# Optimization experiments

Hardware: AMD Instinct MI355X
Metric: run time of the kernel (lower is better)

## Reference

```python
import jax, jax.numpy as jnp
import numpy as np

jax.config.update('jax_enable_x64', True)

NV = 300000
NT = 1200000

# Lookup tables from GshellHelper buffers
TRIANGLE_TABLE = jnp.asarray(np.array([
    [-1, -1, -1, -1, -1, -1], [1, 0, 2, -1, -1, -1], [4, 0, 3, -1, -1, -1],
    [1, 4, 2, 1, 3, 4], [3, 1, 5, -1, -1, -1], [2, 3, 0, 2, 5, 3],
    [1, 4, 0, 1, 5, 4], [4, 2, 5, -1, -1, -1], [4, 5, 2, -1, -1, -1],
    [4, 1, 0, 4, 5, 1], [3, 2, 0, 3, 5, 2], [1, 3, 5, -1, -1, -1],
    [4, 1, 2, 4, 3, 1], [3, 0, 4, -1, -1, -1], [2, 0, 1, -1, -1, -1],
    [-1, -1, -1, -1, -1, -1]], dtype=np.int64))
NUM_TRIANGLES_TABLE = jnp.asarray(np.array([0, 1, 1, 2, 1, 2, 2, 1, 1, 2, 2, 1, 2, 1, 1, 0], dtype=np.int64))
BASE_TET_EDGES = jnp.asarray(np.array([0, 1, 0, 2, 0, 3, 1, 2, 1, 3, 2, 3], dtype=np.int64))


def setup_inputs() -> dict:
    key = jax.random.key(0)
    k1, k2, k3 = jax.random.split(key, 3)
    pos_nx3 = jax.random.normal(k1, (NV, 3), dtype=jnp.float32)
    sdf_n = jax.random.normal(k2, (NV,), dtype=jnp.float32)
    tet_fx4 = jax.random.randint(k3, (NT, 4), 0, NV, dtype=jnp.int64)
    return {'pos_nx3': pos_nx3, 'sdf_n': sdf_n, 'tet_fx4': tet_fx4}


def _marching_tets(pos_nx3, sdf_n, tet_fx4):
    Nv = pos_nx3.shape[0]
    Nt = tet_fx4.shape[0]
    U = Nt * 6  # max possible unique edges (padded, static)
    sentinel = Nv * Nv  # any real edge code is < Nv*Nv

    occ_n = sdf_n > 0                               # [Nv]
    occ_fx4 = occ_n[tet_fx4]                        # [Nt,4]

    # build the 6 edges of every tet and sort each pair (min, max)
    edges = tet_fx4[:, BASE_TET_EDGES].reshape(-1, 2)   # [Nt*6, 2]
    e0 = jnp.minimum(edges[:, 0], edges[:, 1])
    e1 = jnp.maximum(edges[:, 0], edges[:, 1])
    code = e0 * Nv + e1                                  # [Nt*6] int64 edge key

    # dedup edges (torch.unique(..., return_inverse=True) equivalent, padded)
    uniq, inv = jnp.unique(code, size=U, fill_value=sentinel, return_inverse=True)
    u0 = jnp.clip(uniq // Nv, 0, Nv - 1)
    u1 = jnp.clip(uniq % Nv, 0, Nv - 1)
    real = uniq < sentinel
    crossing = real & (occ_n[u0] != occ_n[u1])           # edges with a sign change

    # compacted index for crossing edges; -1 for non-crossing (as in torch mapping)
    mapping = jnp.where(crossing, jnp.cumsum(crossing.astype(jnp.int64)) - 1, -1)
    idx_map = mapping[inv].reshape(Nt, 6)                # [Nt,6]

    # linear interpolation to the zero crossing:
    # verts = (p0 * (-s1) + p1 * s0) / (s0 - s1)   (matches the torch flip/negate math)
    s0 = sdf_n[u0]
    s1 = sdf_n[u1]
    denom = jnp.where(crossing, s0 - s1, jnp.asarray(1.0, sdf_n.dtype))
    v = (pos_nx3[u0] * (-s1 / denom)[:, None] + pos_nx3[u1] * (s0 / denom)[:, None])

    # scatter interpolated verts to their compacted slots; drop non-crossing
    target = jnp.where(crossing, mapping, U)
    verts = jnp.zeros((U, 3), pos_nx3.dtype).at[target].set(v, mode='drop')

    # per-tet sign pattern -> triangle table lookup
    v_id = jnp.asarray([1, 2, 4, 8], dtype=jnp.int64)
    tetindex = (occ_fx4.astype(jnp.int64) * v_id[None, :]).sum(-1)   # [Nt]
    num_triangles = NUM_TRIANGLES_TABLE[tetindex]                     # [Nt] in {0,1,2}
    tri6 = TRIANGLE_TABLE[tetindex]                                   # [Nt,6]
    face_idx = jnp.take_along_axis(idx_map, jnp.clip(tri6, 0, 5), axis=1).reshape(Nt, 2, 3)
    valid_tri = jnp.arange(2, dtype=jnp.int64)[None, :] < num_triangles[:, None]
    faces = jnp.where(valid_tri[:, :, None], face_idx, -1)            # [Nt,2,3], -1 padded

    return verts, faces, num_triangles, crossing


def reference(pos_nx3, sdf_n, tet_fx4):
    return _marching_tets(pos_nx3, sdf_n, tet_fx4)
```

## Files before the change

### kernel.cpp

```cpp
#include <hip/hip_runtime.h>
#include <stdint.h>

typedef unsigned long long u64;
typedef unsigned int u32;

#define NVERT 300000
#define NTET  1200000
#define NE    (NTET*6)
#define TILE  4096
#define NTILES ((NE + TILE - 1)/TILE)
#define IDXBITS 23
#define IDXMASK ((1u<<IDXBITS)-1)
#define CODESHIFT 24
#define NBUCKS 4688
#define BUCKSHIFT 49

#define PK_GRID 512

#define P1_TPB  1024
#define P1_KPT  32
#define P1_KEYS (P1_TPB*P1_KPT)
#define P1_GRID ((NE + P1_KEYS - 1)/P1_KEYS)

#define BSHIFT 16
#define BSZ    65536
#define NBUCK  110
#define BPB    8
#define STAGECAP 2240

#define VERTS_OFF 0
#define FACES_OFF 21600000
#define NUMT_OFF  28800000
#define CROSS_OFF 30000000
#define CODES_ELEM 14000000

__constant__ int c_ea[6] = {0,0,0,1,1,2};
__constant__ int c_eb[6] = {1,2,3,2,3,3};
__constant__ int c_numtri[16] = {0,1,1,2,1,2,2,1,1,2,2,1,2,1,1,0};
__constant__ int c_tritab[16][6] = {
 {-1,-1,-1,-1,-1,-1},{1,0,2,-1,-1,-1},{4,0,3,-1,-1,-1},{1,4,2,1,3,4},
 {3,1,5,-1,-1,-1},{2,3,0,2,5,3},{1,4,0,1,5,4},{4,2,5,-1,-1,-1},
 {4,5,2,-1,-1,-1},{4,1,0,4,5,1},{3,2,0,3,5,2},{1,3,5,-1,-1,-1},
 {4,1,2,4,3,1},{3,0,4,-1,-1,-1},{2,0,1,-1,-1,-1},{-1,-1,-1,-1,-1,-1}};

__device__ __forceinline__ int sw(int j){ return j ^ ((j >> 4) & 15); }

__global__ __launch_bounds__(256) void k_pack(const int* __restrict__ tet, const float* __restrict__ sdf,
                       u64* __restrict__ dst, float* __restrict__ occF, u32* __restrict__ histBlk){
  __shared__ u32 h[NBUCKS];
  __shared__ u64 lk[256*6];
  int tid = threadIdx.x;
  for (int r=tid; r<NBUCKS; r+=256) h[r]=0;
  __syncthreads();
  for (int t0 = blockIdx.x*256; t0 < NTET; t0 += PK_GRID*256){
    int t = t0 + tid;
    if (t < NTET){
      int4 q = ((const int4*)tet)[t];
      int v[4] = {q.x, q.y, q.z, q.w};
      u32 o[4];
      int occ = 0;
      #pragma unroll
      for (int j=0;j<4;j++){ o[j] = sdf[v[j]] > 0.f ? 1u : 0u; occ |= (int)o[j] << j; }
      occF[t] = (float)occ;
      u64 base = (u64)t*6;
      #pragma unroll
      for (int k=0;k<6;k++){
        int a = v[c_ea[k]], b = v[c_eb[k]];
        u64 cross = (o[c_ea[k]] != o[c_eb[k]]) ? 1ull : 0ull;
        int e0 = min(a,b), e1 = max(a,b);
        u64 code = ((u64)e0 << 19) | (u64)e1;
        u64 key = (code << CODESHIFT) | (cross << IDXBITS) | (base + (u64)k);
        lk[tid*6+k] = key;
        atomicAdd(&h[(u32)(key >> BUCKSHIFT)], 1u);
      }
    }
    __syncthreads();
    int nt = NTET - t0; if (nt > 256) nt = 256;
    size_t ob = (size_t)t0*6;
    for (int j=tid; j<nt*6; j+=256) dst[ob + j] = lk[j];
    __syncthreads();
  }
  u32* row = histBlk + (size_t)blockIdx.x * NBUCKS;
  for (int r=tid; r<NBUCKS; r+=256) row[r] = h[r];
}

__global__ void k_reduce_hist(const u32* __restrict__ histBlk, u32* __restrict__ hist){
  int b = blockIdx.x*256 + threadIdx.x;
  if (b >= NBUCKS) return;
  u32 s = 0;
  for (int r=0;r<PK_GRID;r++) s += histBlk[(size_t)r*NBUCKS + b];
  hist[b] = s;
}

__global__ void k_psd(const float* __restrict__ pos, const float* __restrict__ sdf,
                      float4* __restrict__ psd){
  int v = blockIdx.x*blockDim.x + threadIdx.x;
  if (v < NVERT) psd[v] = make_float4(pos[3*v], pos[3*v+1], pos[3*v+2], sdf[v]);
}

__global__ void k_fillm1(float4* __restrict__ p, int n4){
  int i = blockIdx.x*blockDim.x + threadIdx.x;
  if (i < n4) p[i] = make_float4(-1.f,-1.f,-1.f,-1.f);
}

__global__ __launch_bounds__(1024) void k_scan_buckets(const u32* __restrict__ hist,
     u32* __restrict__ boff, u32* __restrict__ gcur){
  __shared__ u32 s[1024];
  int tid = threadIdx.x;
  u32 carry = 0;
  for (int start=0; start<NBUCKS; start+=1024){
    int idx = start + tid;
    u32 x = (idx < NBUCKS) ? hist[idx] : 0;
    s[tid] = x; __syncthreads();
    for (int off=1; off<1024; off<<=1){
      u32 t = (tid >= off) ? s[tid-off] : 0;
      __syncthreads();
      s[tid] += t;
      __syncthreads();
    }
    u32 excl = carry + s[tid] - x;
    if (idx < NBUCKS){ boff[idx] = excl; gcur[idx] = excl; }
    carry += s[1023];
    __syncthreads();
  }
}

__global__ __launch_bounds__(P1_TPB) void k_bucket_scatter(const u64* __restrict__ src,
     u64* __restrict__ dst, u32* __restrict__ gcur){
  __shared__ u32 h[NBUCKS];
  int tid = threadIdx.x;
  for (int r=tid;r<NBUCKS;r+=P1_TPB) h[r]=0;
  __syncthreads();
  size_t gi = (size_t)blockIdx.x*P1_KEYS + (size_t)tid*P1_KPT;
  u64 kk[P1_KPT];
  if (gi + P1_KPT <= NE){
    const ulonglong2* p2 = (const ulonglong2*)(src + gi);
    #pragma unroll
    for (int k2=0;k2<P1_KPT/2;k2++){ ulonglong2 t = p2[k2]; kk[2*k2]=t.x; kk[2*k2+1]=t.y; }
  } else {
    #pragma unroll
    for (int k=0;k<P1_KPT;k++) kk[k] = (gi+k < NE) ? src[gi+k] : ~0ull;
  }
  #pragma unroll
  for (int k=0;k<P1_KPT;k++){
    if (gi+k < NE) atomicAdd(&h[(u32)(kk[k] >> BUCKSHIFT)], 1u);
  }
  __syncthreads();
  for (int r=tid;r<NBUCKS;r+=P1_TPB){
    u32 c = h[r];
    h[r] = c ? atomicAdd(&gcur[r], c) : 0u;
  }
  __syncthreads();
  #pragma unroll
  for (int k=0;k<P1_KPT;k++){
    if (gi+k < NE){
      u32 b = (u32)(kk[k] >> BUCKSHIFT);
      u32 p = atomicAdd(&h[b], 1u);
      dst[p] = kk[k];
    }
  }
}

template<int NK>
__global__ __launch_bounds__(256) void k_sort_bucket(const u64* __restrict__ src,
     u64* __restrict__ dst, const u32* __restrict__ hist, const u32* __restrict__ boff){
  __shared__ u64 keys[NK*256];
  __shared__ u64 wsum[4][2];
  int b = blockIdx.x, tid = threadIdx.x;
  u32 n = hist[b];
  if (n == 0) return;
  if (NK == 4  && n > 1024) return;
  if (NK == 8  && (n <= 1024 || n > 2048)) return;
  if (NK == 12 && (n <= 2048 || n > 3072)) return;
  if (NK == 16 && n <= 3072) return;
  u32 base = boff[b];
  #pragma unroll
  for (int k=0;k<NK;k++){
    int j = k*256 + tid;
    keys[sw(j)] = (j < (int)n) ? src[base + j] : ~0ull;
  }
  __syncthreads();
  int mywave = tid >> 6;
  #pragma unroll 1
  for (int q=0;q<9;q++){
    int sh = 24 + 3*q;
    u64 myk[NK];
    u64 vpack = 0;
    u64 c0 = 0, c1 = 0;
    #pragma unroll
    for (int k=0;k<NK;k++){
      myk[k] = keys[sw(tid*NK+k)];
      u32 d = (u32)((myk[k] >> sh) & 7);
      vpack |= (u64)d << (3*k);
      u64 inc = 1ull << (16*(d&3));
      c0 += (d & 4) ? 0 : inc;
      c1 += (d & 4) ? inc : 0;
    }
    u64 v0 = c0, v1 = c1;
    #pragma unroll
    for (int off=1; off<64; off<<=1){
      u64 t0 = __shfl_up(v0, off, 64);
      u64 t1 = __shfl_up(v1, off, 64);
      if ((tid & 63) >= off){ v0 += t0; v1 += t1; }
    }
    if ((tid & 63) == 63){ wsum[mywave][0] = v0; wsum[mywave][1] = v1; }
    __syncthreads();
    u64 pre0=0, pre1=0, tot0=0, tot1=0;
    #pragma unroll
    for (int wv=0; wv<4; wv++){
      u64 x0 = wsum[wv][0], x1 = wsum[wv][1];
      if (wv < mywave){ pre0 += x0; pre1 += x1; }
      tot0 += x0; tot1 += x1;
    }
    u64 run0 = v0 + pre0 - c0;
    u64 run1 = v1 + pre1 - c1;
    u64 Bp0 = 0, Bp1 = 0;
    u32 acc = 0;
    #pragma unroll
    for (int b2=0;b2<8;b2++){
      u32 f = (u32)(((b2 < 4 ? tot0 : tot1) >> (16*(b2&3))) & 0xFFFF);
      if (b2 < 4) Bp0 |= (u64)acc << (16*b2);
      else        Bp1 |= (u64)acc << (16*(b2&3));
      acc += f;
    }
    #pragma unroll
    for (int k=0;k<NK;k++){
      u32 d = (u32)((vpack >> (3*k)) & 7);
      u32 s2 = d & 3;
      bool hi = (d & 4) != 0;
      u64 Bsel = hi ? Bp1 : Bp0;
      u64 rsel = hi ? run1 : run0;
      u32 pos = (u32)((Bsel >> (16*s2)) & 0xFFFF) + (u32)((rsel >> (16*s2)) & 0xFFFF);
      u64 inc = 1ull << (16*s2);
      run0 += hi ? 0 : inc;
      run1 += hi ? inc : 0;
      keys[sw((int)pos)] = myk[k];
    }
    __syncthreads();
  }
  #pragma unroll
  for (int k=0;k<NK;k++){
    int j = k*256 + tid;
    if (j < (int)n) dst[base + j] = keys[sw(j)];
  }
}

__global__ __launch_bounds__(256) void k_tilesum(const u64* __restrict__ A, u64* __restrict__ tileSums){
  __shared__ u64 s[256];
  int tid = threadIdx.x;
  int start = blockIdx.x*TILE + tid*16;
  u64 myk[16];
  if (start < NE){
    const ulonglong2* A2 = (const ulonglong2*)(A + start);
    #pragma unroll
    for (int k2=0;k2<8;k2++){ ulonglong2 t = A2[k2]; myk[2*k2]=t.x; myk[2*k2+1]=t.y; }
  } else {
    #pragma unroll
    for (int k=0;k<16;k++) myk[k]=0;
  }
  u64 prev = (start > 0 && start <= NE) ? A[start-1] : ~0ull;
  u32 th=0, tc=0;
  #pragma unroll
  for (int k=0;k<16;k++){
    int i = start + k;
    if (i < NE){
      u64 v = myk[k];
      if ((v>>CODESHIFT) != (prev>>CODESHIFT)){
        th++;
        if ((v>>IDXBITS) & 1ull) tc++;
      }
      prev = v;
    }
  }
  s[tid] = ((u64)th<<32) | (u64)tc;
  __syncthreads();
  for (int off=128; off>0; off>>=1){
    if (tid<off) s[tid]+=s[tid+off];
    __syncthreads();
  }
  if (tid==0) tileSums[blockIdx.x] = s[0];
}

__global__ void k_scan_tiles(u64* __restrict__ tileSums, u64* __restrict__ tileOff){
  __shared__ u64 s[256];
  int tid = threadIdx.x;
  u64 carry=0;
  for (int start=0; start<NTILES; start+=256){
    int idx=start+tid;
    u64 x = (idx<NTILES)? tileSums[idx] : 0;
    s[tid]=x; __syncthreads();
    for (int off=1;off<256;off<<=1){
      u64 t=(tid>=off)?s[tid-off]:0;
      __syncthreads();
      s[tid]+=t;
      __syncthreads();
    }
    u64 incl=s[tid], tot=s[255];
    if (idx<NTILES) tileOff[idx] = carry + incl - x;
    carry += tot;
    __syncthreads();
  }
  if (tid==0) tileOff[NTILES] = carry;
}

__global__ __launch_bounds__(256) void k_emit_light(const u64* __restrict__ A,
     const u64* __restrict__ tileOff, u64* __restrict__ pairs, u32* __restrict__ cursors,
     u64* __restrict__ codes, float* __restrict__ crossing_out){
  __shared__ u64 wsum[4];
  __shared__ u32 cnt[NBUCK], lcur[NBUCK];
  __shared__ u32 lofs[NBUCK+1];
  __shared__ u32 gbase[NBUCK];
  __shared__ u64 stage[STAGECAP];
  int tid=threadIdx.x, blk=blockIdx.x;
  int lane = tid & 63, wv = tid >> 6;
  int start = blk*TILE + tid*16;
  if (tid < NBUCK){ cnt[tid]=0; lcur[tid]=0; }
  u64 myk[16];
  if (start < NE){
    const ulonglong2* A2 = (const ulonglong2*)(A + start);
    #pragma unroll
    for (int k2=0;k2<8;k2++){ ulonglong2 t = A2[k2]; myk[2*k2]=t.x; myk[2*k2+1]=t.y; }
  } else {
    #pragma unroll
    for (int k=0;k<16;k++) myk[k]=0;
  }
  u64 prev = (start > 0 && start <= NE) ? A[start-1] : ~0ull;
  u32 headm=0, crossm=0;
  #pragma unroll
  for (int k=0;k<16;k++){
    int i = start + k;
    if (i<NE){
      u64 v = myk[k];
      if ((v>>CODESHIFT) != (prev>>CODESHIFT)) headm |= 1u<<k;
      if ((v>>IDXBITS) & 1ull) crossm |= 1u<<k;
      prev = v;
    }
  }
  __syncthreads();
  #pragma unroll
  for (int k=0;k<16;k++){
    if ((start+k) < NE && ((crossm>>k)&1u))
      atomicAdd(&cnt[((u32)myk[k] & IDXMASK)>>BSHIFT], 1u);
  }
  u32 th = __popc(headm), tc = __popc(headm & crossm);
  u64 x = ((u64)th<<32)|(u64)tc;
  u64 v = x;
  #pragma unroll
  for (int off=1; off<64; off<<=1){
    u64 t = __shfl_up(v, off, 64);
    if (lane >= off) v += t;
  }
  if (lane == 63) wsum[wv] = v;
  __syncthreads();
  u64 pre = 0;
  #pragma unroll
  for (int w2=0; w2<4; w2++){ u64 s2 = wsum[w2]; if (w2 < wv) pre += s2; }
  u64 excl = v - x + pre;
  if (tid < 64){
    u32 a0 = (2*tid   < NBUCK) ? cnt[2*tid]   : 0;
    u32 a1 = (2*tid+1 < NBUCK) ? cnt[2*tid+1] : 0;
    u32 sp = a0 + a1;
    u32 sv = sp;
    #pragma unroll
    for (int off=1; off<64; off<<=1){
      u32 t = __shfl_up(sv, off, 64);
      if (lane >= off) sv += t;
    }
    u32 basex = sv - sp;
    if (2*tid   < NBUCK) lofs[2*tid]   = basex;
    if (2*tid+1 < NBUCK) lofs[2*tid+1] = basex + a0;
    if (tid == 63) lofs[NBUCK] = sv;
  }
  if (tid < NBUCK) gbase[tid] = atomicAdd(&cursors[tid], cnt[tid]);
  __syncthreads();
  bool use_stage = (lofs[NBUCK] <= STAGECAP);
  u64 baseOff = tileOff[blk] + excl;
  u32 H = (u32)(baseOff>>32);
  u32 C = (u32)(baseOff & 0xFFFFFFFFull);
  #pragma unroll
  for (int k=0;k<16;k++){
    int i = start+k;
    if (i>=NE) break;
    bool head  = (headm>>k)&1u;
    bool cross = (crossm>>k)&1u;
    if (head){ H++; if(cross) C++; }
    if (cross){
      int m = (int)C-1;
      u32 orig = (u32)myk[k] & IDXMASK;
      u32 b = orig>>BSHIFT;
      u32 r = atomicAdd(&lcur[b], 1u);
      u64 pr = ((u64)orig<<32) | (u64)(u32)m;
      if (use_stage) stage[lofs[b] + r] = pr;
      else           pairs[(size_t)b*BSZ + gbase[b] + r] = pr;
    }
    if (head){
      crossing_out[H-1] = cross ? 1.f : 0.f;
      if (cross) codes[C-1] = myk[k]>>CODESHIFT;
    }
  }
  __syncthreads();
  if (use_stage){
    int ncross = (int)lofs[NBUCK];
    for (int j = tid; j < ncross; j += 256){
      u64 pr = stage[j];
      u32 b = (u32)(pr>>32) >> BSHIFT;
      pairs[(size_t)b*BSZ + gbase[b] + (u32)(j - (int)lofs[b])] = pr;
    }
  }
}

__global__ __launch_bounds__(256) void k_verts(const u64* __restrict__ codes,
     const float4* __restrict__ psd, const u64* __restrict__ totptr, float* __restrict__ verts){
  __shared__ u64 dummy[5120];
  u32 ncross = (u32)(totptr[0] & 0xFFFFFFFFull);
  u32 stride = gridDim.x * blockDim.x;
  for (u32 i = blockIdx.x*blockDim.x + threadIdx.x; i < ncross; i += stride){
    u64 code = codes[i];
    u32 u0 = (u32)(code >> 19), u1 = (u32)(code & 0x7FFFFull);
    float4 a = psd[u0], b = psd[u1];
    float denom = a.w - b.w;
    float w0 = (-b.w)/denom, w1 = a.w/denom;
    verts[3*i+0] = a.x*w0 + b.x*w1;
    verts[3*i+1] = a.y*w0 + b.y*w1;
    verts[3*i+2] = a.z*w0 + b.z*w1;
  }
  if ((int)ncross < -1){ dummy[threadIdx.x] = codes[0]; verts[0] = (float)dummy[255]; }
}

__global__ void k_tailzero(const u64* __restrict__ totptr,
                           float* __restrict__ verts, float* __restrict__ cross){
  u64 tot = totptr[0];
  u32 nuniq  = (u32)(tot>>32);
  u32 ncross = (u32)(tot & 0xFFFFFFFFull);
  u32 vstart = 3u*ncross;
  u32 vlen = 21600000u - vstart;
  u32 clen = 7200000u - nuniq;
  u32 stride = gridDim.x * blockDim.x;
  for (u32 i = blockIdx.x*blockDim.x + threadIdx.x; i < vlen; i += stride)
    verts[vstart + i] = 0.f;
  for (u32 i = blockIdx.x*blockDim.x + threadIdx.x; i < clen; i += stride)
    cross[nuniq + i] = 0.f;
}

__global__ void k_map_scatter(const u64* __restrict__ pairs, const u32* __restrict__ cursors,
                              float* __restrict__ mapF){
  int b = blockIdx.x / BPB, sub = blockIdx.x % BPB;
  u32 n = cursors[b];
  const u64* p = pairs + (size_t)b*BSZ;
  for (u32 i = (u32)(sub*256 + threadIdx.x); i < n; i += BPB*256){
    u64 v = p[i];
    mapF[(u32)(v>>32)] = (float)(int)(u32)v;
  }
}

__global__ void k_faces(const float* __restrict__ occF, float* faceRegion, float* __restrict__ numt){
  int t = blockIdx.x*blockDim.x + threadIdx.x;
  if (t>=NTET) return;
  int occ = (int)occF[t];
  int ntri = c_numtri[occ];
  float em[6];
  #pragma unroll
  for (int j=0;j<6;j++) em[j] = faceRegion[t*6+j];
  float f[6];
  #pragma unroll
  for (int j=0;j<6;j++){
    int tri = c_tritab[occ][j];
    f[j] = ((j/3) < ntri) ? em[tri] : -1.f;
  }
  #pragma unroll
  for (int j=0;j<6;j++) faceRegion[t*6+j] = f[j];
  numt[t] = (float)ntri;
}

extern "C" void kernel_launch(void* const* d_in, const int* in_sizes, int n_in,
                              void* d_out, int out_size, void* d_ws, size_t ws_size,
                              hipStream_t stream) {
  const float* pos = (const float*)d_in[0];
  const float* sdf = (const float*)d_in[1];
  const int*   tet = (const int*)d_in[2];
  float* out = (float*)d_out;

  char* w = (char*)d_ws;
  u64* bufA     = (u64*)w;
  u32* hist     = (u32*)(w + 57600000);
  u32* boff     = (u32*)(w + 57618752);
  u32* gcur     = (u32*)(w + 57637504);
  u64* tileSums = (u64*)(w + 57656256);
  u64* tileOff  = (u64*)(w + 57670320);
  u32* cursors  = (u32*)(w + 57684392);
  float4* psd   = (float4*)(w + 57684992);
  u64* pairs_ws = (u64*)(w + 62484992);
  u32* histBlk  = (u32*)pairs_ws;

  u64* bufB  = (u64*)d_out;
  u64* codes = (u64*)(out + CODES_ELEM);

  k_pack<<<PK_GRID, 256, 0, stream>>>(tet, sdf, bufA, out + NUMT_OFF, histBlk);
  k_psd<<<(NVERT+255)/256, 256, 0, stream>>>(pos, sdf, psd);
  k_fillm1<<<(7200000/4 + 255)/256, 256, 0, stream>>>((float4*)(out + FACES_OFF), 7200000/4);

  k_reduce_hist<<<(NBUCKS+255)/256, 256, 0, stream>>>(histBlk, hist);
  k_scan_buckets<<<1, 1024, 0, stream>>>(hist, boff, gcur);

  k_bucket_scatter<<<P1_GRID, P1_TPB, 0, stream>>>(bufA, bufB, gcur);
  k_sort_bucket<4><<<NBUCKS, 256, 0, stream>>>(bufB, bufA, hist, boff);
  k_sort_bucket<8><<<NBUCKS, 256, 0, stream>>>(bufB, bufA, hist, boff);
  k_sort_bucket<12><<<NBUCKS, 256, 0, stream>>>(bufB, bufA, hist, boff);
  k_sort_bucket<16><<<NBUCKS, 256, 0, stream>>>(bufB, bufA, hist, boff);

  k_tilesum<<<NTILES, 256, 0, stream>>>(bufA, tileSums);
  k_scan_tiles<<<1, 256, 0, stream>>>(tileSums, tileOff);

  hipMemsetAsync(cursors, 0, NBUCK*sizeof(u32), stream);

  k_emit_light<<<NTILES, 256, 0, stream>>>(bufA, tileOff, pairs_ws, cursors,
                                           codes, out + CROSS_OFF);

  k_verts<<<1024, 256, 0, stream>>>(codes, psd, tileOff + NTILES, out + VERTS_OFF);
  k_tailzero<<<2048, 256, 0, stream>>>(tileOff + NTILES, out + VERTS_OFF, out + CROSS_OFF);

  k_map_scatter<<<NBUCK*BPB, 256, 0, stream>>>(pairs_ws, cursors, out + FACES_OFF);
  k_faces<<<(NTET+255)/256, 256, 0, stream>>>(out + NUMT_OFF, out + FACES_OFF, out + NUMT_OFF);
}
```

Before: 530.7 us.

## Split bucket scatter into coarse and fine two-level radix passes

The single scatter into 4688 buckets is replaced by two passes. A coarse scatter sends keys into 74 super-buckets, then a fine scatter splits each super-bucket into 64 sub-buckets, with 8 blocks per super-bucket. The aim is to cut shared-memory histogram cost and make the global writes better coalesced, since each block now writes to far fewer destinations. The price is an extra full read and write pass over the key array. The per-bucket sorts now run in place on bufA, and the separate kernel that pre-filled the faces buffer with -1 is dropped, which relies on later kernels writing every face slot.

```diff
diff --git a/kernel.cpp b/kernel.cpp
--- a/kernel.cpp
+++ b/kernel.cpp
@@ -14,6 +14,8 @@
 #define CODESHIFT 24
 #define NBUCKS 4688
 #define BUCKSHIFT 49
+#define NCOARSE 74
+#define COARSESHIFT 55
 
 #define PK_GRID 512
 
@@ -21,6 +23,9 @@
 #define P1_KPT  32
 #define P1_KEYS (P1_TPB*P1_KPT)
 #define P1_GRID ((NE + P1_KEYS - 1)/P1_KEYS)
+
+#define FS_SUB 8
+#define FS_CH  32768
 
 #define BSHIFT 16
 #define BSZ    65536
@@ -98,13 +103,8 @@
   if (v < NVERT) psd[v] = make_float4(pos[3*v], pos[3*v+1], pos[3*v+2], sdf[v]);
 }
 
-__global__ void k_fillm1(float4* __restrict__ p, int n4){
-  int i = blockIdx.x*blockDim.x + threadIdx.x;
-  if (i < n4) p[i] = make_float4(-1.f,-1.f,-1.f,-1.f);
-}
-
 __global__ __launch_bounds__(1024) void k_scan_buckets(const u32* __restrict__ hist,
-     u32* __restrict__ boff, u32* __restrict__ gcur){
+     u32* __restrict__ boff, u32* __restrict__ gcur, u32* __restrict__ ccur){
   __shared__ u32 s[1024];
   int tid = threadIdx.x;
   u32 carry = 0;
@@ -119,17 +119,20 @@
       __syncthreads();
     }
     u32 excl = carry + s[tid] - x;
-    if (idx < NBUCKS){ boff[idx] = excl; gcur[idx] = excl; }
+    if (idx < NBUCKS){
+      boff[idx] = excl; gcur[idx] = excl;
+      if ((idx & 63) == 0) ccur[idx >> 6] = excl;
+    }
     carry += s[1023];
     __syncthreads();
   }
 }
 
-__global__ __launch_bounds__(P1_TPB) void k_bucket_scatter(const u64* __restrict__ src,
-     u64* __restrict__ dst, u32* __restrict__ gcur){
-  __shared__ u32 h[NBUCKS];
+__global__ __launch_bounds__(P1_TPB) void k_coarse_scatter(const u64* __restrict__ src,
+     u64* __restrict__ dst, u32* __restrict__ ccur){
+  __shared__ u32 h[NCOARSE];
   int tid = threadIdx.x;
-  for (int r=tid;r<NBUCKS;r+=P1_TPB) h[r]=0;
+  if (tid < NCOARSE) h[tid]=0;
   __syncthreads();
   size_t gi = (size_t)blockIdx.x*P1_KEYS + (size_t)tid*P1_KPT;
   u64 kk[P1_KPT];
@@ -143,21 +146,57 @@
   }
   #pragma unroll
   for (int k=0;k<P1_KPT;k++){
-    if (gi+k < NE) atomicAdd(&h[(u32)(kk[k] >> BUCKSHIFT)], 1u);
-  }
-  __syncthreads();
-  for (int r=tid;r<NBUCKS;r+=P1_TPB){
-    u32 c = h[r];
-    h[r] = c ? atomicAdd(&gcur[r], c) : 0u;
+    if (gi+k < NE) atomicAdd(&h[(u32)(kk[k] >> COARSESHIFT)], 1u);
+  }
+  __syncthreads();
+  if (tid < NCOARSE){
+    u32 c = h[tid];
+    h[tid] = c ? atomicAdd(&ccur[tid], c) : 0u;
   }
   __syncthreads();
   #pragma unroll
   for (int k=0;k<P1_KPT;k++){
     if (gi+k < NE){
-      u32 b = (u32)(kk[k] >> BUCKSHIFT);
+      u32 b = (u32)(kk[k] >> COARSESHIFT);
       u32 p = atomicAdd(&h[b], 1u);
       dst[p] = kk[k];
     }
+  }
+}
+
+__global__ __launch_bounds__(P1_TPB) void k_fine_scatter(const u64* __restrict__ src,
+     u64* __restrict__ dst, const u32* __restrict__ boff, u32* __restrict__ gcur){
+  __shared__ u32 h[64];
+  __shared__ u32 rb[64];
+  int c = blockIdx.x >> 3, sub = blockIdx.x & (FS_SUB-1);
+  int tid = threadIdx.x;
+  u32 startc = boff[c*64];
+  u32 endc = (c == NCOARSE-1) ? (u32)NE : boff[(c+1)*64];
+  u32 size = endc - startc;
+  u32 shareLen = (size + FS_SUB - 1) / FS_SUB;
+  u32 s0 = startc + sub*shareLen;
+  u32 s1 = s0 + shareLen; if (s1 > endc) s1 = endc;
+  if (s0 >= s1) return;
+  for (u32 base = s0; base < s1; base += FS_CH){
+    u32 lim = base + FS_CH; if (lim > s1) lim = s1;
+    if (tid < 64) h[tid] = 0;
+    __syncthreads();
+    for (u32 i = base + tid; i < lim; i += P1_TPB)
+      atomicAdd(&h[(u32)(src[i] >> BUCKSHIFT) & 63u], 1u);
+    __syncthreads();
+    if (tid < 64){
+      u32 cc = h[tid];
+      rb[tid] = cc ? atomicAdd(&gcur[c*64 + tid], cc) : 0u;
+      h[tid] = 0;
+    }
+    __syncthreads();
+    for (u32 i = base + tid; i < lim; i += P1_TPB){
+      u64 v = src[i];
+      u32 f = (u32)(v >> BUCKSHIFT) & 63u;
+      u32 p = rb[f] + atomicAdd(&h[f], 1u);
+      dst[p] = v;
+    }
+    __syncthreads();
   }
 }
 
@@ -488,8 +527,9 @@
   u64* tileSums = (u64*)(w + 57656256);
   u64* tileOff  = (u64*)(w + 57670320);
   u32* cursors  = (u32*)(w + 57684392);
-  float4* psd   = (float4*)(w + 57684992);
-  u64* pairs_ws = (u64*)(w + 62484992);
+  u32* ccur     = (u32*)(w + 57684832);
+  float4* psd   = (float4*)(w + 57685504);
+  u64* pairs_ws = (u64*)(w + 62485504);
   u32* histBlk  = (u32*)pairs_ws;
 
   u64* bufB  = (u64*)d_out;
@@ -497,16 +537,17 @@
 
   k_pack<<<PK_GRID, 256, 0, stream>>>(tet, sdf, bufA, out + NUMT_OFF, histBlk);
   k_psd<<<(NVERT+255)/256, 256, 0, stream>>>(pos, sdf, psd);
-  k_fillm1<<<(7200000/4 + 255)/256, 256, 0, stream>>>((float4*)(out + FACES_OFF), 7200000/4);
 
   k_reduce_hist<<<(NBUCKS+255)/256, 256, 0, stream>>>(histBlk, hist);
-  k_scan_buckets<<<1, 1024, 0, stream>>>(hist, boff, gcur);
-
-  k_bucket_scatter<<<P1_GRID, P1_TPB, 0, stream>>>(bufA, bufB, gcur);
-  k_sort_bucket<4><<<NBUCKS, 256, 0, stream>>>(bufB, bufA, hist, boff);
-  k_sort_bucket<8><<<NBUCKS, 256, 0, stream>>>(bufB, bufA, hist, boff);
-  k_sort_bucket<12><<<NBUCKS, 256, 0, stream>>>(bufB, bufA, hist, boff);
-  k_sort_bucket<16><<<NBUCKS, 256, 0, stream>>>(bufB, bufA, hist, boff);
+  k_scan_buckets<<<1, 1024, 0, stream>>>(hist, boff, gcur, ccur);
+
+  k_coarse_scatter<<<P1_GRID, P1_TPB, 0, stream>>>(bufA, bufB, ccur);
+  k_fine_scatter<<<NCOARSE*FS_SUB, P1_TPB, 0, stream>>>(bufB, bufA, boff, gcur);
+
+  k_sort_bucket<4><<<NBUCKS, 256, 0, stream>>>(bufA, bufA, hist, boff);
+  k_sort_bucket<8><<<NBUCKS, 256, 0, stream>>>(bufA, bufA, hist, boff);
+  k_sort_bucket<12><<<NBUCKS, 256, 0, stream>>>(bufA, bufA, hist, boff);
+  k_sort_bucket<16><<<NBUCKS, 256, 0, stream>>>(bufA, bufA, hist, boff);
 
   k_tilesum<<<NTILES, 256, 0, stream>>>(bufA, tileSums);
   k_scan_tiles<<<1, 256, 0, stream>>>(tileSums, tileOff);
```

New measurement: 522.1 us. No clear change (-1.6%).
